# Kernel tuning notes

Measured on AMD Instinct MI355X. Metric: run time of the kernel, lower is better.

## Reference

```python
import jax, jax.numpy as jnp
import numpy as np

K = 8               # top-k frequencies
PRED_LEN = 96       # prediction_length
LOW_FREQ = 1        # low_frequency cutoff (drops DC)


def setup_inputs() -> dict:
    key = jax.random.key(0)
    x = jax.random.normal(key, (32, 2048, 64), dtype=jnp.float32)
    return {"x": x}


def reference(x):
    b, t, d = x.shape
    x_freq = jnp.fft.rfft(x, axis=1)                 # (b, t//2+1, d) complex
    freqs = jnp.fft.rfftfreq(t).astype(x.dtype)
    if t % 2 == 0:
        x_freq = x_freq[:, LOW_FREQ:-1]              # drop DC and Nyquist
        f = freqs[LOW_FREQ:-1]
    else:
        x_freq = x_freq[:, LOW_FREQ:]
        f = freqs[LOW_FREQ:]

    # top-k over frequency dim (axis=1), independently per (b, d)
    mag = jnp.abs(x_freq)                            # (b, F, d)
    _, idx = jax.lax.top_k(jnp.moveaxis(mag, 1, 2), K)  # (b, d, K), sorted desc
    idx = jnp.moveaxis(idx, 1, 2)                    # (b, K, d)
    x_k = jnp.take_along_axis(x_freq, idx, axis=1)   # (b, K, d) complex
    f_k = f[idx]                                     # (b, K, d)

    # extrapolate: add conjugate (negative) frequencies, then cos-sum
    x2 = jnp.concatenate([x_k, jnp.conj(x_k)], axis=1)  # (b, 2K, d)
    f2 = jnp.concatenate([f_k, -f_k], axis=1)           # (b, 2K, d)
    t_val = jnp.arange(t + PRED_LEN, dtype=x.dtype)     # (T,)
    amp = jnp.abs(x2) / t                               # (b, 2K, d)
    phase = jnp.angle(x2)                               # (b, 2K, d)
    # (b, 2K, T, d) broadcast intermediate, reduced over freq axis
    x_time = amp[:, :, None, :] * jnp.cos(
        2.0 * np.float32(np.pi) * f2[:, :, None, :] * t_val[None, None, :, None]
        + phase[:, :, None, :]
    )
    return x_time.sum(axis=1)                        # (b, t+PRED_LEN, d)
```

## Files before the change

kernel.cpp:

```cpp
#include <hip/hip_runtime.h>
#include <math.h>

#define BB 32
#define TT 2048
#define DD 64
#define PRED 96
#define TP (TT + PRED)
#define KTOP 8
#define MARGIN 8e-4f
#define PI_D 3.14159265358979323846

__device__ __forceinline__ int br6(int l) { return (int)(__brev((unsigned)l) >> 26); }
static constexpr int BR5[32] = {0,16,8,24,4,20,12,28,2,18,10,26,6,22,14,30,
                                1,17,9,25,5,21,13,29,3,19,11,27,7,23,15,31};
static constexpr float C32T[16] = {
    1.0f, 0.98078528040323044913f, 0.92387953251128675613f, 0.83146961230254523708f,
    0.70710678118654752440f, 0.55557023301960222474f, 0.38268343236508977173f, 0.19509032201612826785f,
    0.0f, -0.19509032201612826785f, -0.38268343236508977173f, -0.55557023301960222474f,
    -0.70710678118654752440f, -0.83146961230254523708f, -0.92387953251128675613f, -0.98078528040323044913f};
static constexpr float S32T[16] = {
    0.0f, 0.19509032201612826785f, 0.38268343236508977173f, 0.55557023301960222474f,
    0.70710678118654752440f, 0.83146961230254523708f, 0.92387953251128675613f, 0.98078528040323044913f,
    1.0f, 0.98078528040323044913f, 0.92387953251128675613f, 0.83146961230254523708f,
    0.70710678118654752440f, 0.55557023301960222474f, 0.38268343236508977173f, 0.19509032201612826785f};

__device__ __forceinline__ float2 ctw(float2 a, int m) {
    const float rev = (float)m * (1.0f / 2048.0f);
    const float c = __builtin_amdgcn_cosf(rev);
    const float s = __builtin_amdgcn_sinf(rev);
    return make_float2(a.x * c + a.y * s, a.y * c - a.x * s);
}

#define SRE(w,a) POOL[(w) * 2112 + (a)]
#define SIM(w,a) POOL[8448 + (w) * 2112 + (a)]
#define TILE(tv,d8) POOL[(tv) * 8 + (d8)]

__global__ __launch_bounds__(256) void fused_kernel(const float* __restrict__ x,
                                                    float* __restrict__ out) {
    __shared__ float POOL[17152];
    __shared__ int   coefK[8][KTOP];
    __shared__ float coefR[8][KTOP], coefI[8][KTOP];

    const int t    = threadIdx.x;
    const int wv   = t >> 6, lane = t & 63;
    const int bid  = blockIdx.x;
    const int xcd  = bid & 7;
    const int idx  = bid >> 3;
    const int b    = xcd * 4 + (idx >> 3);
    const int grp  = idx & 7;
    const int dp   = grp * 4 + wv;
    const int d_base = grp * 8;

    const float2* xv = (const float2*)x;
    const size_t xbase = (size_t)b * TT * (DD / 2) + dp;

    float2 v[32];
    #pragma unroll
    for (int i = 0; i < 32; ++i)
        v[i] = xv[xbase + (size_t)(64 * BR5[i] + lane) * (DD / 2)];

    #pragma unroll
    for (int s = 1; s <= 5; ++s) {
        const int m = 1 << s, half = m >> 1, stepw = 32 >> s;
        #pragma unroll
        for (int g = 0; g < 32; g += m) {
            #pragma unroll
            for (int j = 0; j < half; ++j) {
                const float c = C32T[j * stepw], sn = S32T[j * stepw];
                const int i0 = g + j, i1 = i0 + half;
                const float tr = c * v[i1].x + sn * v[i1].y;
                const float ti = c * v[i1].y - sn * v[i1].x;
                v[i1] = make_float2(v[i0].x - tr, v[i0].y - ti);
                v[i0] = make_float2(v[i0].x + tr, v[i0].y + ti);
            }
        }
    }

    #pragma unroll
    for (int q = 1; q < 32; ++q) v[q] = ctw(v[q], (lane * q) & (TT - 1));

    {
        const int rl = br6(lane);
        #pragma unroll
        for (int q = 0; q < 32; ++q) {
            v[q].x = __shfl(v[q].x, rl, 64);
            v[q].y = __shfl(v[q].y, rl, 64);
        }
    }
    #pragma unroll
    for (int s = 1; s <= 6; ++s) {
        const int half = 1 << (s - 1);
        const float rev = (float)(lane & (half - 1)) / (float)(1 << s);
        const float wc  = __builtin_amdgcn_cosf(rev);
        const float wsn = __builtin_amdgcn_sinf(rev);
        const bool  hi  = (lane & half) != 0;
        #pragma unroll
        for (int q = 0; q < 32; ++q) {
            float2 pv;
            pv.x = __shfl_xor(v[q].x, half, 64);
            pv.y = __shfl_xor(v[q].y, half, 64);
            const float2 bsv = hi ? v[q] : pv;
            const float2 asv = hi ? pv : v[q];
            const float tr = wc * bsv.x + wsn * bsv.y;
            const float ti = wc * bsv.y - wsn * bsv.x;
            v[q] = hi ? make_float2(asv.x - tr, asv.y - ti)
                      : make_float2(asv.x + tr, asv.y + ti);
        }
    }

    #pragma unroll
    for (int q = 0; q < 32; ++q) {
        const int a = 33 * lane + q;
        SRE(wv, a) = v[q].x;
        SIM(wv, a) = v[q].y;
    }

    const int sig = lane >> 5, hl = lane & 31;
    unsigned A[32];
    #pragma unroll
    for (int q = 0; q < 32; ++q) {
        const int k = 32 * hl + q;
        unsigned kk = 0u;
        if (k != 0) {
            const int a1 = k + (k >> 5);
            const int pk = TT - k, a2 = pk + (pk >> 5);
            const float zr = SRE(wv, a1), zi = SIM(wv, a1);
            const float yr = SRE(wv, a2), yi = SIM(wv, a2);
            float cr, ci;
            if (sig == 0) { cr = 0.5f * (zr + yr); ci = 0.5f * (zi - yi); }
            else          { cr = 0.5f * (zi + yi); ci = 0.5f * (yr - zr); }
            const float mg = cr * cr + ci * ci;
            kk = (__float_as_uint(mg) & 0xFFFFF800u) | (unsigned)(2047 - k);
        }
        A[q] = kk;
    }

    #pragma unroll
    for (int sz = 2; sz <= 32; sz <<= 1) {
        #pragma unroll
        for (int d = sz >> 1; d > 0; d >>= 1) {
            #pragma unroll
            for (int i2 = 0; i2 < 32; ++i2) {
                const int j2i = i2 ^ d;
                if (j2i > i2) {
                    const bool desc = ((i2 & sz) == 0);
                    const unsigned a = A[i2], b2 = A[j2i];
                    const unsigned mx = a > b2 ? a : b2, mn = a > b2 ? b2 : a;
                    A[i2] = desc ? mx : mn;  A[j2i] = desc ? mn : mx;
                }
            }
        }
    }
    #pragma unroll
    for (int off = 1; off <= 16; off <<= 1) {
        unsigned Bv[16];
        #pragma unroll
        for (int i2 = 0; i2 < 16; ++i2)
            Bv[i2] = (unsigned)__shfl_xor((int)A[i2], off, 64);
        #pragma unroll
        for (int i2 = 0; i2 < 16; ++i2) {
            const unsigned o = Bv[15 - i2];
            A[i2] = A[i2] > o ? A[i2] : o;
        }
        #pragma unroll
        for (int d = 8; d > 0; d >>= 1) {
            #pragma unroll
            for (int i2 = 0; i2 < 16; ++i2) {
                if ((i2 & d) == 0) {
                    const int j2i = i2 + d;
                    const unsigned a = A[i2], b2 = A[j2i];
                    A[i2] = a > b2 ? a : b2;  A[j2i] = a > b2 ? b2 : a;
                }
            }
        }
    }

    const float m8f = __uint_as_float(A[7] & 0xFFFFF800u);
    unsigned bandmask = 0u;
    #pragma unroll
    for (int r = 0; r < 16; ++r) {
        const float mr = __uint_as_float(A[r] & 0xFFFFF800u);
        if (fabsf(mr - m8f) <= MARGIN * m8f) bandmask |= (1u << r);
    }
    const int flg = (bandmask != (1u << 7)) ? 1 : 0;

    unsigned myk = 0u;
    #pragma unroll
    for (int i2 = 0; i2 < 16; ++i2) myk = (hl == i2) ? A[i2] : myk;
    const int kcand = 2047 - (int)(myk & 0x7FFu);
    const int s_local = 2 * wv + sig;

    if (!flg && hl < KTOP) {
        const int k = kcand, a1 = k + (k >> 5), pk = TT - k, a2 = pk + (pk >> 5);
        const float zr = SRE(wv, a1), zi = SIM(wv, a1);
        const float yr = SRE(wv, a2), yi = SIM(wv, a2);
        float cr, ci;
        if (sig == 0) { cr = 0.5f * (zr + yr); ci = 0.5f * (zi - yi); }
        else          { cr = 0.5f * (zi + yi); ci = 0.5f * (yr - zr); }
        coefK[s_local][hl] = k;
        coefR[s_local][hl] = cr * (2.0f / (float)TT);
        coefI[s_local][hl] = ci * (2.0f / (float)TT);
    }

    const int flg0 = __shfl(flg, 0, 64);
    const int flg1 = __shfl(flg, 32, 64);

    if (flg0 | flg1) {
        float2 sv[32];
        #pragma unroll
        for (int m = 0; m < 32; ++m)
            sv[m] = xv[xbase + (size_t)(lane + 64 * m) * (DD / 2)];
        const double thA = -2.0 * PI_D * (double)lane / 64.0;
        const double thB = -2.0 * PI_D * (double)lane / (double)TT;
        const double wac = cos(thA), was = sin(thA);
        const double wbc = cos(thB), wbs = sin(thB);

        for (int sg = 0; sg < 2; ++sg) {
            const int flg_s = (sg == 0) ? flg0 : flg1;
            if (!flg_s) continue;
            const unsigned bm = (unsigned)__shfl((int)bandmask, 32 * sg, 64);
            const int lo = (int)__builtin_ctz(bm);
            double myM = 0.0, myR = 0.0, myI = 0.0;
            for (int r = 0; r < 16; ++r) {
                if (!((bm >> r) & 1u)) continue;
                const int kr = __shfl(kcand, 32 * sg + r, 64);
                double ar = 0.0, ai = 0.0;
                for (int m = 0; m < 32; ++m) {
                    const int n  = lane + 64 * m;
                    const int mm = (n * kr) & (TT - 1);
                    const double qc  = __shfl(wac, mm >> 5, 64);
                    const double qs  = __shfl(was, mm >> 5, 64);
                    const double rc2 = __shfl(wbc, mm & 31, 64);
                    const double rs2 = __shfl(wbs, mm & 31, 64);
                    const double wr = qc * rc2 - qs * rs2;
                    const double wi = qc * rs2 + qs * rc2;
                    const double xs = (sg == 0) ? (double)sv[m].x : (double)sv[m].y;
                    ar = fma(xs, wr, ar);
                    ai = fma(xs, wi, ai);
                }
                #pragma unroll
                for (int off = 32; off; off >>= 1) {
                    ar += __shfl_xor(ar, off, 64);
                    ai += __shfl_xor(ai, off, 64);
                }
                if (lane == 32 * sg + r) { myM = ar * ar + ai * ai; myR = ar; myI = ai; }
            }
            const int h16 = hl & 15;
            const double selfM = __shfl(myM, 32 * sg + h16, 64);
            const int    selfK = __shfl(kcand, 32 * sg + h16, 64);
            int rb = 0;
            for (int r2 = 0; r2 < 16; ++r2) {
                if (!((bm >> r2) & 1u)) continue;
                const double om = __shfl(myM, 32 * sg + r2, 64);
                const int    ok = __shfl(kcand, 32 * sg + r2, 64);
                if (r2 != h16 && (om > selfM || (om == selfM && ok < selfK))) ++rb;
            }
            const int isband = (int)((bm >> h16) & 1u);
            const int rank = isband ? (lo + rb) : h16;
            if (sig == sg && hl < 16 && rank < KTOP) {
                coefK[s_local][rank] = kcand;
                if (isband) {
                    coefR[s_local][rank] = (float)(myR * (2.0 / (double)TT));
                    coefI[s_local][rank] = (float)(myI * (2.0 / (double)TT));
                } else {
                    const int k = kcand, a1 = k + (k >> 5), pk = TT - k, a2 = pk + (pk >> 5);
                    const float zr = SRE(wv, a1), zi = SIM(wv, a1);
                    const float yr = SRE(wv, a2), yi = SIM(wv, a2);
                    float cr, ci;
                    if (sg == 0) { cr = 0.5f * (zr + yr); ci = 0.5f * (zi - yi); }
                    else          { cr = 0.5f * (zi + yi); ci = 0.5f * (yr - zr); }
                    coefR[s_local][rank] = cr * (2.0f / (float)TT);
                    coefI[s_local][rank] = ci * (2.0f / (float)TT);
                }
            }
        }
    }
    __syncthreads();

    const int d8 = t & 7, tq = t >> 3;
    int   kc[KTOP];
    float fr[KTOP], fi[KTOP], pc[KTOP], ps[KTOP], rc[KTOP], rs[KTOP];
    #pragma unroll
    for (int p = 0; p < KTOP; ++p) {
        kc[p] = coefK[d8][p];
        fr[p] = coefR[d8][p];
        fi[p] = coefI[d8][p];
        const int j0 = (kc[p] * tq) & (TT - 1);
        const float rv0 = (float)j0 * (1.0f / 2048.0f);
        pc[p] = __builtin_amdgcn_cosf(rv0);
        ps[p] = __builtin_amdgcn_sinf(rv0);
        const int jr = (kc[p] * 32) & (TT - 1);
        const float rvr = (float)jr * (1.0f / 2048.0f);
        rc[p] = __builtin_amdgcn_cosf(rvr);
        rs[p] = __builtin_amdgcn_sinf(rvr);
    }
    #pragma unroll 4
    for (int m = 0; m < 67; ++m) {
        const int tv = tq + 32 * m;
        float acc = 0.0f;
        #pragma unroll
        for (int p = 0; p < KTOP; ++p) acc += fr[p] * pc[p] - fi[p] * ps[p];
        TILE(tv, d8) = acc;
        #pragma unroll
        for (int p = 0; p < KTOP; ++p) {
            const float nc = pc[p] * rc[p] - ps[p] * rs[p];
            const float ns = pc[p] * rs[p] + ps[p] * rc[p];
            pc[p] = nc; ps[p] = ns;
        }
    }
    __syncthreads();

    float* ob = out + (size_t)b * TP * DD + d_base;
    for (int it = 0; it < 67; ++it) {
        const int f  = it * 256 + t;
        const int dd = f & 7, tv = f >> 3;
        ob[(size_t)tv * DD + dd] = POOL[f];
    }
}

extern "C" void kernel_launch(void* const* d_in, const int* in_sizes, int n_in,
                              void* d_out, int out_size, void* d_ws, size_t ws_size,
                              hipStream_t stream) {
    const float* x = (const float*)d_in[0];
    float* out = (float*)d_out;
    (void)d_ws; (void)ws_size; (void)in_sizes; (void)n_in; (void)out_size;

    fused_kernel<<<BB * 8, 256, 0, stream>>>(x, out);
}
```

Measured before the change: 110.9 us.

## Split each 2048-point FFT across two wavefronts and double the grid

Each complex signal pair is now transformed by two wavefronts with 16 values per lane instead of one wavefront holding 32, and the final radix-2 stage is exchanged through LDS. The grid doubles to 512 blocks of 4 channels each, with launch bounds asking for 2 blocks per CU. This is meant to cut register pressure and raise occupancy and parallelism. The output is now written straight to global memory with 4-wide strided stores instead of being staged in an LDS tile, which may reduce store coalescing.

```diff
diff --git a/kernel.cpp b/kernel.cpp
--- a/kernel.cpp
+++ b/kernel.cpp
@@ -11,8 +11,7 @@
 #define PI_D 3.14159265358979323846
 
 __device__ __forceinline__ int br6(int l) { return (int)(__brev((unsigned)l) >> 26); }
-static constexpr int BR5[32] = {0,16,8,24,4,20,12,28,2,18,10,26,6,22,14,30,
-                                1,17,9,25,5,21,13,29,3,19,11,27,7,23,15,31};
+static constexpr int BR4[16] = {0,8,4,12,2,10,6,14,1,9,5,13,3,11,7,15};
 static constexpr float C32T[16] = {
     1.0f, 0.98078528040323044913f, 0.92387953251128675613f, 0.83146961230254523708f,
     0.70710678118654752440f, 0.55557023301960222474f, 0.38268343236508977173f, 0.19509032201612826785f,
@@ -31,39 +30,40 @@
     return make_float2(a.x * c + a.y * s, a.y * c - a.x * s);
 }
 
-#define SRE(w,a) POOL[(w) * 2112 + (a)]
-#define SIM(w,a) POOL[8448 + (w) * 2112 + (a)]
-#define TILE(tv,d8) POOL[(tv) * 8 + (d8)]
-
-__global__ __launch_bounds__(256) void fused_kernel(const float* __restrict__ x,
-                                                    float* __restrict__ out) {
-    __shared__ float POOL[17152];
-    __shared__ int   coefK[8][KTOP];
-    __shared__ float coefR[8][KTOP], coefI[8][KTOP];
+#define SRE(pr,a) POOL[9216 + (pr) * 4224 + (a)]
+#define SIM(pr,a) POOL[9216 + (pr) * 4224 + 2112 + (a)]
+
+__global__ __launch_bounds__(256, 2) void fused_kernel(const float* __restrict__ x,
+                                                       float* __restrict__ out) {
+    __shared__ float POOL[17664];
+    __shared__ int   coefK[4][KTOP];
+    __shared__ float coefR[4][KTOP], coefI[4][KTOP];
 
     const int t    = threadIdx.x;
-    const int wv   = t >> 6, lane = t & 63;
+    const int wv   = t >> 6, p = t & 63;
+    const int pair = wv >> 1, w = wv & 1;
     const int bid  = blockIdx.x;
     const int xcd  = bid & 7;
     const int idx  = bid >> 3;
-    const int b    = xcd * 4 + (idx >> 3);
-    const int grp  = idx & 7;
-    const int dp   = grp * 4 + wv;
-    const int d_base = grp * 8;
+    const int b    = (idx >> 3) * 4 + (xcd >> 1);
+    const int grp4 = (xcd & 1) * 8 + (idx & 7);
+    const int dp   = grp4 * 2 + pair;
+    const int ch   = grp4 * 4 + wv;
 
     const float2* xv = (const float2*)x;
     const size_t xbase = (size_t)b * TT * (DD / 2) + dp;
-
-    float2 v[32];
-    #pragma unroll
-    for (int i = 0; i < 32; ++i)
-        v[i] = xv[xbase + (size_t)(64 * BR5[i] + lane) * (DD / 2)];
-
-    #pragma unroll
-    for (int s = 1; s <= 5; ++s) {
+    const int rl = 2 * br6(p) + w;
+
+    float2 v[16];
+    #pragma unroll
+    for (int i = 0; i < 16; ++i)
+        v[i] = xv[xbase + (size_t)(128 * BR4[i] + rl) * (DD / 2)];
+
+    #pragma unroll
+    for (int s = 1; s <= 4; ++s) {
         const int m = 1 << s, half = m >> 1, stepw = 32 >> s;
         #pragma unroll
-        for (int g = 0; g < 32; g += m) {
+        for (int g = 0; g < 16; g += m) {
             #pragma unroll
             for (int j = 0; j < half; ++j) {
                 const float c = C32T[j * stepw], sn = S32T[j * stepw];
@@ -77,25 +77,17 @@
     }
 
     #pragma unroll
-    for (int q = 1; q < 32; ++q) v[q] = ctw(v[q], (lane * q) & (TT - 1));
-
-    {
-        const int rl = br6(lane);
-        #pragma unroll
-        for (int q = 0; q < 32; ++q) {
-            v[q].x = __shfl(v[q].x, rl, 64);
-            v[q].y = __shfl(v[q].y, rl, 64);
-        }
-    }
+    for (int q = 1; q < 16; ++q) v[q] = ctw(v[q], (rl * q) & (TT - 1));
+
     #pragma unroll
     for (int s = 1; s <= 6; ++s) {
         const int half = 1 << (s - 1);
-        const float rev = (float)(lane & (half - 1)) / (float)(1 << s);
+        const float rev = (float)(p & (half - 1)) / (float)(1 << s);
         const float wc  = __builtin_amdgcn_cosf(rev);
         const float wsn = __builtin_amdgcn_sinf(rev);
-        const bool  hi  = (lane & half) != 0;
-        #pragma unroll
-        for (int q = 0; q < 32; ++q) {
+        const bool  hi  = (p & half) != 0;
+        #pragma unroll
+        for (int q = 0; q < 16; ++q) {
             float2 pv;
             pv.x = __shfl_xor(v[q].x, half, 64);
             pv.y = __shfl_xor(v[q].y, half, 64);
@@ -108,27 +100,52 @@
         }
     }
 
-    #pragma unroll
-    for (int q = 0; q < 32; ++q) {
-        const int a = 33 * lane + q;
-        SRE(wv, a) = v[q].x;
-        SIM(wv, a) = v[q].y;
-    }
-
-    const int sig = lane >> 5, hl = lane & 31;
-    unsigned A[32];
-    #pragma unroll
-    for (int q = 0; q < 32; ++q) {
-        const int k = 32 * hl + q;
+    {
+        const int exw = pair * 4608 + w * 2304 + p * 36;
+        #pragma unroll
+        for (int c = 0; c < 8; ++c)
+            *(float4*)&POOL[exw + 4 * c] =
+                make_float4(v[2*c].x, v[2*c].y, v[2*c+1].x, v[2*c+1].y);
+    }
+    __syncthreads();
+    {
+        const int exr = pair * 4608 + (1 - w) * 2304 + p * 36;
+        const float revp = (float)p * (1.0f / 128.0f);
+        const float wc7 = __builtin_amdgcn_cosf(revp);
+        const float ws7 = __builtin_amdgcn_sinf(revp);
+        const int kb = 1024 * w + 16 * p;
+        #pragma unroll
+        for (int c = 0; c < 8; ++c) {
+            const float4 g = *(const float4*)&POOL[exr + 4 * c];
+            #pragma unroll
+            for (int e = 0; e < 2; ++e) {
+                const int q = 2 * c + e;
+                const float2 pv = e ? make_float2(g.z, g.w) : make_float2(g.x, g.y);
+                const float2 bsv = w ? v[q] : pv;
+                const float2 asv = w ? pv : v[q];
+                const float tr = wc7 * bsv.x + ws7 * bsv.y;
+                const float ti = wc7 * bsv.y - ws7 * bsv.x;
+                const int k = kb + q, a = k + (k >> 5);
+                SRE(pair, a) = w ? (asv.x - tr) : (asv.x + tr);
+                SIM(pair, a) = w ? (asv.y - ti) : (asv.y + ti);
+            }
+        }
+    }
+    __syncthreads();
+
+    unsigned A[16];
+    #pragma unroll
+    for (int q = 0; q < 16; ++q) {
+        const int k = 16 * p + q;
         unsigned kk = 0u;
         if (k != 0) {
             const int a1 = k + (k >> 5);
             const int pk = TT - k, a2 = pk + (pk >> 5);
-            const float zr = SRE(wv, a1), zi = SIM(wv, a1);
-            const float yr = SRE(wv, a2), yi = SIM(wv, a2);
+            const float zr = SRE(pair, a1), zi = SIM(pair, a1);
+            const float yr = SRE(pair, a2), yi = SIM(pair, a2);
             float cr, ci;
-            if (sig == 0) { cr = 0.5f * (zr + yr); ci = 0.5f * (zi - yi); }
-            else          { cr = 0.5f * (zi + yi); ci = 0.5f * (yr - zr); }
+            if (w == 0) { cr = 0.5f * (zr + yr); ci = 0.5f * (zi - yi); }
+            else        { cr = 0.5f * (zi + yi); ci = 0.5f * (yr - zr); }
             const float mg = cr * cr + ci * ci;
             kk = (__float_as_uint(mg) & 0xFFFFF800u) | (unsigned)(2047 - k);
         }
@@ -136,11 +153,11 @@
     }
 
     #pragma unroll
-    for (int sz = 2; sz <= 32; sz <<= 1) {
+    for (int sz = 2; sz <= 16; sz <<= 1) {
         #pragma unroll
         for (int d = sz >> 1; d > 0; d >>= 1) {
             #pragma unroll
-            for (int i2 = 0; i2 < 32; ++i2) {
+            for (int i2 = 0; i2 < 16; ++i2) {
                 const int j2i = i2 ^ d;
                 if (j2i > i2) {
                     const bool desc = ((i2 & sz) == 0);
@@ -152,7 +169,7 @@
         }
     }
     #pragma unroll
-    for (int off = 1; off <= 16; off <<= 1) {
+    for (int off = 1; off <= 32; off <<= 1) {
         unsigned Bv[16];
         #pragma unroll
         for (int i2 = 0; i2 < 16; ++i2)
@@ -186,135 +203,120 @@
 
     unsigned myk = 0u;
     #pragma unroll
-    for (int i2 = 0; i2 < 16; ++i2) myk = (hl == i2) ? A[i2] : myk;
+    for (int i2 = 0; i2 < 16; ++i2) myk = (p == i2) ? A[i2] : myk;
     const int kcand = 2047 - (int)(myk & 0x7FFu);
-    const int s_local = 2 * wv + sig;
-
-    if (!flg && hl < KTOP) {
+
+    if (!flg && p < KTOP) {
         const int k = kcand, a1 = k + (k >> 5), pk = TT - k, a2 = pk + (pk >> 5);
-        const float zr = SRE(wv, a1), zi = SIM(wv, a1);
-        const float yr = SRE(wv, a2), yi = SIM(wv, a2);
+        const float zr = SRE(pair, a1), zi = SIM(pair, a1);
+        const float yr = SRE(pair, a2), yi = SIM(pair, a2);
         float cr, ci;
-        if (sig == 0) { cr = 0.5f * (zr + yr); ci = 0.5f * (zi - yi); }
-        else          { cr = 0.5f * (zi + yi); ci = 0.5f * (yr - zr); }
-        coefK[s_local][hl] = k;
-        coefR[s_local][hl] = cr * (2.0f / (float)TT);
-        coefI[s_local][hl] = ci * (2.0f / (float)TT);
-    }
-
-    const int flg0 = __shfl(flg, 0, 64);
-    const int flg1 = __shfl(flg, 32, 64);
-
-    if (flg0 | flg1) {
-        float2 sv[32];
-        #pragma unroll
-        for (int m = 0; m < 32; ++m)
-            sv[m] = xv[xbase + (size_t)(lane + 64 * m) * (DD / 2)];
-        const double thA = -2.0 * PI_D * (double)lane / 64.0;
-        const double thB = -2.0 * PI_D * (double)lane / (double)TT;
+        if (w == 0) { cr = 0.5f * (zr + yr); ci = 0.5f * (zi - yi); }
+        else        { cr = 0.5f * (zi + yi); ci = 0.5f * (yr - zr); }
+        coefK[wv][p] = k;
+        coefR[wv][p] = cr * (2.0f / (float)TT);
+        coefI[wv][p] = ci * (2.0f / (float)TT);
+    }
+
+    if (flg) {
+        float sv[32];
+        const float* xs = x + (size_t)b * TT * DD + ch;
+        #pragma unroll
+        for (int m2 = 0; m2 < 32; ++m2)
+            sv[m2] = xs[(size_t)(p + 64 * m2) * DD];
+        const double thA = -2.0 * PI_D * (double)p / 64.0;
+        const double thB = -2.0 * PI_D * (double)p / (double)TT;
         const double wac = cos(thA), was = sin(thA);
         const double wbc = cos(thB), wbs = sin(thB);
 
-        for (int sg = 0; sg < 2; ++sg) {
-            const int flg_s = (sg == 0) ? flg0 : flg1;
-            if (!flg_s) continue;
-            const unsigned bm = (unsigned)__shfl((int)bandmask, 32 * sg, 64);
-            const int lo = (int)__builtin_ctz(bm);
-            double myM = 0.0, myR = 0.0, myI = 0.0;
-            for (int r = 0; r < 16; ++r) {
-                if (!((bm >> r) & 1u)) continue;
-                const int kr = __shfl(kcand, 32 * sg + r, 64);
-                double ar = 0.0, ai = 0.0;
-                for (int m = 0; m < 32; ++m) {
-                    const int n  = lane + 64 * m;
-                    const int mm = (n * kr) & (TT - 1);
-                    const double qc  = __shfl(wac, mm >> 5, 64);
-                    const double qs  = __shfl(was, mm >> 5, 64);
-                    const double rc2 = __shfl(wbc, mm & 31, 64);
-                    const double rs2 = __shfl(wbs, mm & 31, 64);
-                    const double wr = qc * rc2 - qs * rs2;
-                    const double wi = qc * rs2 + qs * rc2;
-                    const double xs = (sg == 0) ? (double)sv[m].x : (double)sv[m].y;
-                    ar = fma(xs, wr, ar);
-                    ai = fma(xs, wi, ai);
-                }
-                #pragma unroll
-                for (int off = 32; off; off >>= 1) {
-                    ar += __shfl_xor(ar, off, 64);
-                    ai += __shfl_xor(ai, off, 64);
-                }
-                if (lane == 32 * sg + r) { myM = ar * ar + ai * ai; myR = ar; myI = ai; }
-            }
-            const int h16 = hl & 15;
-            const double selfM = __shfl(myM, 32 * sg + h16, 64);
-            const int    selfK = __shfl(kcand, 32 * sg + h16, 64);
-            int rb = 0;
-            for (int r2 = 0; r2 < 16; ++r2) {
-                if (!((bm >> r2) & 1u)) continue;
-                const double om = __shfl(myM, 32 * sg + r2, 64);
-                const int    ok = __shfl(kcand, 32 * sg + r2, 64);
-                if (r2 != h16 && (om > selfM || (om == selfM && ok < selfK))) ++rb;
-            }
-            const int isband = (int)((bm >> h16) & 1u);
-            const int rank = isband ? (lo + rb) : h16;
-            if (sig == sg && hl < 16 && rank < KTOP) {
-                coefK[s_local][rank] = kcand;
-                if (isband) {
-                    coefR[s_local][rank] = (float)(myR * (2.0 / (double)TT));
-                    coefI[s_local][rank] = (float)(myI * (2.0 / (double)TT));
-                } else {
-                    const int k = kcand, a1 = k + (k >> 5), pk = TT - k, a2 = pk + (pk >> 5);
-                    const float zr = SRE(wv, a1), zi = SIM(wv, a1);
-                    const float yr = SRE(wv, a2), yi = SIM(wv, a2);
-                    float cr, ci;
-                    if (sg == 0) { cr = 0.5f * (zr + yr); ci = 0.5f * (zi - yi); }
-                    else          { cr = 0.5f * (zi + yi); ci = 0.5f * (yr - zr); }
-                    coefR[s_local][rank] = cr * (2.0f / (float)TT);
-                    coefI[s_local][rank] = ci * (2.0f / (float)TT);
-                }
+        const unsigned bm = bandmask;
+        const int lo = (int)__builtin_ctz(bm);
+        double myM = 0.0, myR = 0.0, myI = 0.0;
+        for (int r = 0; r < 16; ++r) {
+            if (!((bm >> r) & 1u)) continue;
+            const int kr = __shfl(kcand, r, 64);
+            double ar = 0.0, ai = 0.0;
+            for (int m2 = 0; m2 < 32; ++m2) {
+                const int n  = p + 64 * m2;
+                const int mm = (n * kr) & (TT - 1);
+                const double qc  = __shfl(wac, mm >> 5, 64);
+                const double qs  = __shfl(was, mm >> 5, 64);
+                const double rc2 = __shfl(wbc, mm & 31, 64);
+                const double rs2 = __shfl(wbs, mm & 31, 64);
+                const double wr = qc * rc2 - qs * rs2;
+                const double wi = qc * rs2 + qs * rc2;
+                ar = fma((double)sv[m2], wr, ar);
+                ai = fma((double)sv[m2], wi, ai);
+            }
+            #pragma unroll
+            for (int off = 32; off; off >>= 1) {
+                ar += __shfl_xor(ar, off, 64);
+                ai += __shfl_xor(ai, off, 64);
+            }
+            if (p == r) { myM = ar * ar + ai * ai; myR = ar; myI = ai; }
+        }
+        const int h16 = p & 15;
+        const double selfM = __shfl(myM, h16, 64);
+        const int    selfK = __shfl(kcand, h16, 64);
+        int rb = 0;
+        for (int r2 = 0; r2 < 16; ++r2) {
+            if (!((bm >> r2) & 1u)) continue;
+            const double om = __shfl(myM, r2, 64);
+            const int    ok = __shfl(kcand, r2, 64);
+            if (r2 != h16 && (om > selfM || (om == selfM && ok < selfK))) ++rb;
+        }
+        const int isband = (int)((bm >> h16) & 1u);
+        const int rank = isband ? (lo + rb) : h16;
+        if (p < 16 && rank < KTOP) {
+            coefK[wv][rank] = kcand;
+            if (isband) {
+                coefR[wv][rank] = (float)(myR * (2.0 / (double)TT));
+                coefI[wv][rank] = (float)(myI * (2.0 / (double)TT));
+            } else {
+                const int k = kcand, a1 = k + (k >> 5), pk = TT - k, a2 = pk + (pk >> 5);
+                const float zr = SRE(pair, a1), zi = SIM(pair, a1);
+                const float yr = SRE(pair, a2), yi = SIM(pair, a2);
+                float cr, ci;
+                if (w == 0) { cr = 0.5f * (zr + yr); ci = 0.5f * (zi - yi); }
+                else        { cr = 0.5f * (zi + yi); ci = 0.5f * (yr - zr); }
+                coefR[wv][rank] = cr * (2.0f / (float)TT);
+                coefI[wv][rank] = ci * (2.0f / (float)TT);
             }
         }
     }
     __syncthreads();
 
-    const int d8 = t & 7, tq = t >> 3;
+    const int d4 = t & 3, tq = t >> 2;
     int   kc[KTOP];
     float fr[KTOP], fi[KTOP], pc[KTOP], ps[KTOP], rc[KTOP], rs[KTOP];
     #pragma unroll
-    for (int p = 0; p < KTOP; ++p) {
-        kc[p] = coefK[d8][p];
-        fr[p] = coefR[d8][p];
-        fi[p] = coefI[d8][p];
-        const int j0 = (kc[p] * tq) & (TT - 1);
+    for (int pp = 0; pp < KTOP; ++pp) {
+        kc[pp] = coefK[d4][pp];
+        fr[pp] = coefR[d4][pp];
+        fi[pp] = coefI[d4][pp];
+        const int j0 = (kc[pp] * tq) & (TT - 1);
         const float rv0 = (float)j0 * (1.0f / 2048.0f);
-        pc[p] = __builtin_amdgcn_cosf(rv0);
-        ps[p] = __builtin_amdgcn_sinf(rv0);
-        const int jr = (kc[p] * 32) & (TT - 1);
+        pc[pp] = __builtin_amdgcn_cosf(rv0);
+        ps[pp] = __builtin_amdgcn_sinf(rv0);
+        const int jr = (kc[pp] * 64) & (TT - 1);
         const float rvr = (float)jr * (1.0f / 2048.0f);
-        rc[p] = __builtin_amdgcn_cosf(rvr);
-        rs[p] = __builtin_amdgcn_sinf(rvr);
-    }
-    #pragma unroll 4
-    for (int m = 0; m < 67; ++m) {
-        const int tv = tq + 32 * m;
+        rc[pp] = __builtin_amdgcn_cosf(rvr);
+        rs[pp] = __builtin_amdgcn_sinf(rvr);
+    }
+    float* ob = out + (size_t)b * TP * DD + grp4 * 4 + d4;
+    #pragma unroll 2
+    for (int m = 0; m < 34; ++m) {
+        const int tv = tq + 64 * m;
         float acc = 0.0f;
         #pragma unroll
-        for (int p = 0; p < KTOP; ++p) acc += fr[p] * pc[p] - fi[p] * ps[p];
-        TILE(tv, d8) = acc;
-        #pragma unroll
-        for (int p = 0; p < KTOP; ++p) {
-            const float nc = pc[p] * rc[p] - ps[p] * rs[p];
-            const float ns = pc[p] * rs[p] + ps[p] * rc[p];
-            pc[p] = nc; ps[p] = ns;
-        }
-    }
-    __syncthreads();
-
-    float* ob = out + (size_t)b * TP * DD + d_base;
-    for (int it = 0; it < 67; ++it) {
-        const int f  = it * 256 + t;
-        const int dd = f & 7, tv = f >> 3;
-        ob[(size_t)tv * DD + dd] = POOL[f];
+        for (int pp = 0; pp < KTOP; ++pp) acc += fr[pp] * pc[pp] - fi[pp] * ps[pp];
+        if (tv < TP) ob[(size_t)tv * DD] = acc;
+        #pragma unroll
+        for (int pp = 0; pp < KTOP; ++pp) {
+            const float nc = pc[pp] * rc[pp] - ps[pp] * rs[pp];
+            const float ns = pc[pp] * rs[pp] + ps[pp] * rc[pp];
+            pc[pp] = nc; ps[pp] = ns;
+        }
     }
 }
 
@@ -325,5 +327,5 @@
     float* out = (float*)d_out;
     (void)d_ws; (void)ws_size; (void)in_sizes; (void)n_in; (void)out_size;
 
-    fused_kernel<<<BB * 8, 256, 0, stream>>>(x, out);
+    fused_kernel<<<BB * 16, 256, 0, stream>>>(x, out);
 }
```

Result: faster. 97.47 us (-12.1%).
